# Kernel optimization log

Measured on AMD Instinct MI355X. Metric: run time of the kernel, lower is better.

The kernel has to match this reference:

```python
import jax, jax.numpy as jnp
import numpy as np

B, S, D_IN, D_OUT, H = 4, 2048, 1024, 1024, 16
HD = D_OUT // H


def setup_inputs() -> dict:
    key = jax.random.key(0)
    ks = jax.random.split(key, 6)
    s_in = 1.0 / np.sqrt(D_IN)
    s_out = 1.0 / np.sqrt(D_OUT)
    return {
        "x": jax.random.normal(ks[0], (B, S, D_IN), dtype=jnp.float32),
        "Wq": jax.random.uniform(ks[1], (D_IN, D_OUT), jnp.float32, -s_in, s_in),
        "Wk": jax.random.uniform(ks[2], (D_IN, D_OUT), jnp.float32, -s_in, s_in),
        "Wv": jax.random.uniform(ks[3], (D_IN, D_OUT), jnp.float32, -s_in, s_in),
        "Wo": jax.random.uniform(ks[4], (D_OUT, D_OUT), jnp.float32, -s_out, s_out),
        "bo": jax.random.uniform(ks[5], (D_OUT,), jnp.float32, -s_out, s_out),
    }


def reference(x, Wq, Wk, Wv, Wo, bo):
    b, s, _ = x.shape
    # project and split heads: (b, h, s, hd)
    def heads(w):
        return (x @ w).reshape(b, s, H, HD).transpose(0, 2, 1, 3)
    q, k, v = heads(Wq), heads(Wk), heads(Wv)
    scores = jnp.einsum("bhqd,bhkd->bhqk", q, k) / np.sqrt(HD).astype(np.float32)
    causal = jnp.tril(jnp.ones((s, s), dtype=bool))  # True = keep
    scores = jnp.where(causal, scores, -jnp.inf)
    attn = jax.nn.softmax(scores, axis=-1)
    ctx = jnp.einsum("bhqk,bhkd->bhqd", attn, v)
    ctx = ctx.transpose(0, 2, 1, 3).reshape(b, s, D_OUT)
    return ctx @ Wo.T + bo
```

## Files before the change

kernel.cpp:

```cpp
#include <hip/hip_runtime.h>
#include <hip/hip_bf16.h>

#define BB   4
#define SS   2048
#define DIN  1024
#define DOUT 1024
#define NH   16
#define HDIM 64

typedef __hip_bfloat16 bf16;
typedef __attribute__((ext_vector_type(8))) short short8;
typedef __attribute__((ext_vector_type(4))) float floatx4;

#define AS1(p) ((const __attribute__((address_space(1))) void*)(p))
#define AS3(p) ((__attribute__((address_space(3))) void*)(p))

__global__ void cast_f32_bf16_kernel(const float* __restrict__ src, bf16* __restrict__ dst) {
    size_t i = ((size_t)blockIdx.x * 256 + threadIdx.x) * 8;
    float4 a = *(const float4*)(src + i);
    float4 b = *(const float4*)(src + i + 4);
    bf16 o[8] __attribute__((aligned(16)));
    o[0] = __float2bfloat16(a.x); o[1] = __float2bfloat16(a.y);
    o[2] = __float2bfloat16(a.z); o[3] = __float2bfloat16(a.w);
    o[4] = __float2bfloat16(b.x); o[5] = __float2bfloat16(b.y);
    o[6] = __float2bfloat16(b.z); o[7] = __float2bfloat16(b.w);
    *(short8*)(dst + i) = *(short8*)o;
}

__global__ void prep_wqkv_kernel(const float* __restrict__ Wq, const float* __restrict__ Wk,
                                 const float* __restrict__ Wv, bf16* __restrict__ wt) {
    __shared__ float tile[64][65];
    const int kt = blockIdx.x;
    const int nt = blockIdx.y;
    const int k0 = kt * 64, n0 = nt * 64;
    const float* W = (n0 < 1024) ? Wq : (n0 < 2048 ? Wk : Wv);
    const int col0 = n0 & 1023;
    const int tid = threadIdx.x;
    {
        const int kl = tid >> 2, nc = (tid & 3) * 16;
        const float* src = W + (size_t)(k0 + kl) * 1024 + col0 + nc;
        #pragma unroll
        for (int i = 0; i < 16; i += 4) {
            float4 v = *(const float4*)(src + i);
            tile[kl][nc + i + 0] = v.x; tile[kl][nc + i + 1] = v.y;
            tile[kl][nc + i + 2] = v.z; tile[kl][nc + i + 3] = v.w;
        }
    }
    __syncthreads();
    {
        const int nl = tid >> 2, kc = (tid & 3) * 16;
        bf16 o[16] __attribute__((aligned(16)));
        #pragma unroll
        for (int i = 0; i < 16; ++i) o[i] = __float2bfloat16(tile[kc + i][nl]);
        bf16* dst = wt + (size_t)(n0 + nl) * 1024 + k0 + kc;
        *(short8*)dst       = *(short8*)&o[0];
        *(short8*)(dst + 8) = *(short8*)&o[8];
    }
}

template<int EPI>
__global__ __launch_bounds__(256) void gemm_bt_kernel(
    const bf16* __restrict__ A, const bf16* __restrict__ Bt,
    void* __restrict__ C, const float* __restrict__ bias, int K, int ldc) {
    __shared__ __align__(16) bf16 As[128][32];
    __shared__ __align__(16) bf16 Bs[128][32];
    const int tid  = threadIdx.x;
    const int wave = tid >> 6, lane = tid & 63;
    const int lm   = lane & 15, quad = lane >> 4;
    const int wm   = (wave >> 1) * 64, wn = (wave & 1) * 64;
    const size_t rowA0 = (size_t)blockIdx.x * 128;
    const size_t rowB0 = (size_t)blockIdx.y * 128;
    const int srow = wave * 16 + (lane >> 2);
    const int skc  = (lane & 3) * 8;

    floatx4 acc[4][4] = {};

    for (int k0 = 0; k0 < K; k0 += 32) {
        __syncthreads();
        #pragma unroll
        for (int r = 0; r < 2; ++r) {
            const bf16* gA = A  + (rowA0 + r * 64 + srow) * (size_t)K + k0 + skc;
            __builtin_amdgcn_global_load_lds(AS1(gA), AS3(&As[r * 64 + wave * 16][0]), 16, 0, 0);
            const bf16* gB = Bt + (rowB0 + r * 64 + srow) * (size_t)K + k0 + skc;
            __builtin_amdgcn_global_load_lds(AS1(gB), AS3(&Bs[r * 64 + wave * 16][0]), 16, 0, 0);
        }
        __syncthreads();
        short8 a[4], b[4];
        #pragma unroll
        for (int i = 0; i < 4; ++i) a[i] = *(const short8*)&As[wm + i * 16 + lm][quad * 8];
        #pragma unroll
        for (int j = 0; j < 4; ++j) b[j] = *(const short8*)&Bs[wn + j * 16 + lm][quad * 8];
        #pragma unroll
        for (int i = 0; i < 4; ++i)
            #pragma unroll
            for (int j = 0; j < 4; ++j)
                acc[i][j] = __builtin_amdgcn_mfma_f32_16x16x32_bf16(a[i], b[j], acc[i][j], 0, 0, 0);
    }

    #pragma unroll
    for (int i = 0; i < 4; ++i) {
        size_t row = rowA0 + wm + i * 16 + quad * 4;
        #pragma unroll
        for (int j = 0; j < 4; ++j) {
            size_t col = rowB0 + wn + j * 16 + lm;
            float bv = (EPI == 1) ? bias[col] : 0.0f;
            #pragma unroll
            for (int r = 0; r < 4; ++r) {
                if (EPI == 0)
                    ((bf16*)C)[(row + r) * ldc + col] = __float2bfloat16(acc[i][j][r]);
                else
                    ((float*)C)[(row + r) * ldc + col] = acc[i][j][r] + bv;
            }
        }
    }
}

__global__ void transpose_v_kernel(const bf16* __restrict__ qkv, bf16* __restrict__ vt) {
    __shared__ __align__(16) bf16 tile[64][72];
    const int st = blockIdx.x;
    const int bh = blockIdx.y;
    const int b = bh >> 4, h = bh & 15;
    const int s0 = st * 64;
    const int tid = threadIdx.x;
    {
        const int sl = tid >> 2, hc = (tid & 3) * 16;
        const bf16* src = qkv + ((size_t)(b * SS + s0 + sl)) * 3072 + 2048 + h * 64 + hc;
        *(short8*)&tile[sl][hc]     = *(const short8*)src;
        *(short8*)&tile[sl][hc + 8] = *(const short8*)(src + 8);
    }
    __syncthreads();
    {
        const int hl = tid >> 2, sc = (tid & 3) * 16;
        bf16 o[16] __attribute__((aligned(16)));
        #pragma unroll
        for (int i = 0; i < 16; ++i) o[i] = tile[sc + i][hl];
        bf16* dst = vt + ((size_t)(bh * 64 + hl)) * SS + s0 + sc;
        *(short8*)dst       = *(short8*)&o[0];
        *(short8*)(dst + 8) = *(short8*)&o[8];
    }
}

#define PSTR 68
__global__ __launch_bounds__(256, 2) void flash_attn_kernel(
    const bf16* __restrict__ qkv, const bf16* __restrict__ vt, bf16* __restrict__ ctx) {
    __shared__ __align__(16) bf16 Ks[64 * 64];
    __shared__ __align__(16) bf16 Vs[64 * 64];
    __shared__ __align__(16) bf16 Pl[4][32 * PSTR + 8];
    const int tid  = threadIdx.x;
    const int wave = tid >> 6, lane = tid & 63;
    const int lm   = lane & 15, quad = lane >> 4;

    const int id  = blockIdx.x;
    const int j   = id >> 3;
    const int bh  = (id & 7) * 8 + (j & 7);
    const int p0  = j >> 3;
    const int b = bh >> 4, h = bh & 15;

    const int lane8r = lane >> 3;
    const int schunk = (lane & 7) ^ lane8r;

    bf16* Pw = &Pl[wave][0];

    #pragma unroll 1
    for (int ph = 0; ph < 2; ++ph) {
        const int p = ph ? (15 - p0) : p0;
        const int qb = p * 128 + wave * 32;
        const int nkt = 2 * p + 2;

        short8 bq[2][2];
        #pragma unroll
        for (int g = 0; g < 2; ++g) {
            const bf16* qp = qkv + ((size_t)(b * SS + qb + g * 16 + lm)) * 3072 + h * 64 + quad * 8;
            bq[g][0] = *(const short8*)qp;
            bq[g][1] = *(const short8*)(qp + 32);
        }

        floatx4 o[2][4] = {};
        float lsum[2] = {0.f, 0.f};

        #pragma unroll 1
        for (int kt = 0; kt < nkt; ++kt) {
            __syncthreads();
            #pragma unroll
            for (int c = 0; c < 2; ++c) {
                const int row = c * 32 + wave * 8 + lane8r;
                const bf16* gk = qkv + ((size_t)(b * SS + kt * 64 + row)) * 3072 + 1024 + h * 64 + schunk * 8;
                __builtin_amdgcn_global_load_lds(AS1(gk), AS3(Ks + (c * 256 + wave * 64) * 8), 16, 0, 0);
                const bf16* gv = vt + ((size_t)((b * NH + h) * 64 + row)) * SS + kt * 64 + schunk * 8;
                __builtin_amdgcn_global_load_lds(AS1(gv), AS3(Vs + (c * 256 + wave * 64) * 8), 16, 0, 0);
            }
            __syncthreads();

            const int sw = lm & 7;
            short8 ka[4][2], va[4][2];
            #pragma unroll
            for (int nt = 0; nt < 4; ++nt) {
                const int r0 = (nt * 16 + lm) * 64;
                ka[nt][0] = *(const short8*)(Ks + r0 + ((quad ^ sw) * 8));
                ka[nt][1] = *(const short8*)(Ks + r0 + (((4 + quad) ^ sw) * 8));
                va[nt][0] = *(const short8*)(Vs + r0 + ((quad ^ sw) * 8));
                va[nt][1] = *(const short8*)(Vs + r0 + (((4 + quad) ^ sw) * 8));
            }

            #pragma unroll
            for (int g = 0; g < 2; ++g) {
                floatx4 sc[4];
                #pragma unroll
                for (int nt = 0; nt < 4; ++nt) {
                    floatx4 z = {};
                    z = __builtin_amdgcn_mfma_f32_16x16x32_bf16(ka[nt][0], bq[g][0], z, 0, 0, 0);
                    z = __builtin_amdgcn_mfma_f32_16x16x32_bf16(ka[nt][1], bq[g][1], z, 0, 0, 0);
                    sc[nt] = z;
                }
                if (kt * 64 + 63 > qb + g * 16) {
                    const int qrow = qb + g * 16 + lm;
                    #pragma unroll
                    for (int nt = 0; nt < 4; ++nt)
                        #pragma unroll
                        for (int r = 0; r < 4; ++r)
                            if (kt * 64 + nt * 16 + quad * 4 + r > qrow) sc[nt][r] = -1e30f;
                }
                #pragma unroll
                for (int nt = 0; nt < 4; ++nt) {
                    bf16 pk[4] __attribute__((aligned(8)));
                    #pragma unroll
                    for (int r = 0; r < 4; ++r) {
                        float pv = __builtin_amdgcn_exp2f(sc[nt][r] * 0.18033688f);
                        lsum[g] += pv;
                        pk[r] = __float2bfloat16(pv);
                    }
                    *(uint64_t*)&Pw[(g * 16 + lm) * PSTR + nt * 16 + quad * 4] = *(uint64_t*)pk;
                }
            }
            #pragma unroll
            for (int g = 0; g < 2; ++g) {
                const short8 ap0 = *(const short8*)&Pw[(g * 16 + lm) * PSTR + quad * 8];
                const short8 ap1 = *(const short8*)&Pw[(g * 16 + lm) * PSTR + 32 + quad * 8];
                #pragma unroll
                for (int t = 0; t < 4; ++t) {
                    o[g][t] = __builtin_amdgcn_mfma_f32_16x16x32_bf16(ap0, va[t][0], o[g][t], 0, 0, 0);
                    o[g][t] = __builtin_amdgcn_mfma_f32_16x16x32_bf16(ap1, va[t][1], o[g][t], 0, 0, 0);
                }
            }
        }

        #pragma unroll
        for (int g = 0; g < 2; ++g) {
            float rsum = lsum[g];
            rsum += __shfl_xor(rsum, 16);
            rsum += __shfl_xor(rsum, 32);
            float rl[4];
            #pragma unroll
            for (int r = 0; r < 4; ++r) rl[r] = 1.0f / __shfl(rsum, quad * 4 + r);
            #pragma unroll
            for (int t = 0; t < 4; ++t)
                #pragma unroll
                for (int r = 0; r < 4; ++r) {
                    size_t row = (size_t)b * SS + qb + g * 16 + quad * 4 + r;
                    ctx[row * 1024 + h * 64 + t * 16 + lm] = __float2bfloat16(o[g][t][r] * rl[r]);
                }
        }
    }
}

extern "C" void kernel_launch(void* const* d_in, const int* in_sizes, int n_in,
                              void* d_out, int out_size, void* d_ws, size_t ws_size,
                              hipStream_t stream) {
    const float* x  = (const float*)d_in[0];
    const float* Wq = (const float*)d_in[1];
    const float* Wk = (const float*)d_in[2];
    const float* Wv = (const float*)d_in[3];
    const float* Wo = (const float*)d_in[4];
    const float* bo = (const float*)d_in[5];

    char* ws = (char*)d_ws;
    bf16* xb  = (bf16*)ws;  ws += (size_t)8192 * 1024 * 2;
    bf16* wt  = (bf16*)ws;  ws += (size_t)3072 * 1024 * 2;
    bf16* wob = (bf16*)ws;  ws += (size_t)1024 * 1024 * 2;
    bf16* qkv = (bf16*)ws;  ws += (size_t)8192 * 3072 * 2;
    bf16* vtb = (bf16*)ws;  ws += (size_t)BB * NH * HDIM * SS * 2;
    bf16* ctx = xb;

    cast_f32_bf16_kernel<<<4096, 256, 0, stream>>>(x, xb);
    prep_wqkv_kernel<<<dim3(16, 48), 256, 0, stream>>>(Wq, Wk, Wv, wt);
    cast_f32_bf16_kernel<<<512, 256, 0, stream>>>(Wo, wob);
    gemm_bt_kernel<0><<<dim3(64, 24), 256, 0, stream>>>(xb, wt, (void*)qkv, nullptr, 1024, 3072);
    transpose_v_kernel<<<dim3(32, 64), 256, 0, stream>>>(qkv, vtb);
    flash_attn_kernel<<<512, 256, 0, stream>>>(qkv, vtb, ctx);
    gemm_bt_kernel<1><<<dim3(64, 8), 256, 0, stream>>>(ctx, wob, d_out, bo, 1024, 1024);
}
```

Before: 273.5 us.

## Double-buffer K/V tiles in LDS and prefetch next tile during compute

Adds a second LDS buffer for the K and V tiles in the flash attention kernel. The first tile is loaded before the loop, and each iteration issues async global-to-LDS loads for the next tile before computing on the current one. This hides global load latency behind the MFMA work and drops one barrier per iteration. In exchange it doubles K/V LDS usage and relies on the compiler placing the correct wait counters before the barrier for the async LDS loads.

```diff
diff --git a/kernel.cpp b/kernel.cpp
--- a/kernel.cpp
+++ b/kernel.cpp
@@ -143,8 +143,8 @@
 #define PSTR 68
 __global__ __launch_bounds__(256, 2) void flash_attn_kernel(
     const bf16* __restrict__ qkv, const bf16* __restrict__ vt, bf16* __restrict__ ctx) {
-    __shared__ __align__(16) bf16 Ks[64 * 64];
-    __shared__ __align__(16) bf16 Vs[64 * 64];
+    __shared__ __align__(16) bf16 Ks[2][64 * 64];
+    __shared__ __align__(16) bf16 Vs[2][64 * 64];
     __shared__ __align__(16) bf16 Pl[4][32 * PSTR + 8];
     const int tid  = threadIdx.x;
     const int wave = tid >> 6, lane = tid & 63;
@@ -159,6 +159,9 @@
     const int lane8r = lane >> 3;
     const int schunk = (lane & 7) ^ lane8r;
 
+    const bf16* kg = qkv + (size_t)b * SS * 3072 + 1024 + h * 64 + schunk * 8;
+    const bf16* vg = vt + (size_t)(b * NH + h) * 64 * SS + schunk * 8;
+
     bf16* Pw = &Pl[wave][0];
 
     #pragma unroll 1
@@ -178,28 +181,40 @@
         floatx4 o[2][4] = {};
         float lsum[2] = {0.f, 0.f};
 
+        if (ph) __syncthreads();
+        #pragma unroll
+        for (int c = 0; c < 2; ++c) {
+            const int row = c * 32 + wave * 8 + lane8r;
+            __builtin_amdgcn_global_load_lds(AS1(kg + (size_t)row * 3072), AS3(&Ks[0][(c * 256 + wave * 64) * 8]), 16, 0, 0);
+            __builtin_amdgcn_global_load_lds(AS1(vg + (size_t)row * SS), AS3(&Vs[0][(c * 256 + wave * 64) * 8]), 16, 0, 0);
+        }
+
         #pragma unroll 1
         for (int kt = 0; kt < nkt; ++kt) {
+            const int cur = kt & 1;
             __syncthreads();
-            #pragma unroll
-            for (int c = 0; c < 2; ++c) {
-                const int row = c * 32 + wave * 8 + lane8r;
-                const bf16* gk = qkv + ((size_t)(b * SS + kt * 64 + row)) * 3072 + 1024 + h * 64 + schunk * 8;
-                __builtin_amdgcn_global_load_lds(AS1(gk), AS3(Ks + (c * 256 + wave * 64) * 8), 16, 0, 0);
-                const bf16* gv = vt + ((size_t)((b * NH + h) * 64 + row)) * SS + kt * 64 + schunk * 8;
-                __builtin_amdgcn_global_load_lds(AS1(gv), AS3(Vs + (c * 256 + wave * 64) * 8), 16, 0, 0);
-            }
-            __syncthreads();
+            if (kt + 1 < nkt) {
+                #pragma unroll
+                for (int c = 0; c < 2; ++c) {
+                    const int row = c * 32 + wave * 8 + lane8r;
+                    __builtin_amdgcn_global_load_lds(AS1(kg + (size_t)((kt + 1) * 64 + row) * 3072),
+                                                     AS3(&Ks[cur ^ 1][(c * 256 + wave * 64) * 8]), 16, 0, 0);
+                    __builtin_amdgcn_global_load_lds(AS1(vg + (size_t)row * SS + (kt + 1) * 64),
+                                                     AS3(&Vs[cur ^ 1][(c * 256 + wave * 64) * 8]), 16, 0, 0);
+                }
+            }
 
             const int sw = lm & 7;
+            const bf16* Ksb = &Ks[cur][0];
+            const bf16* Vsb = &Vs[cur][0];
             short8 ka[4][2], va[4][2];
             #pragma unroll
             for (int nt = 0; nt < 4; ++nt) {
                 const int r0 = (nt * 16 + lm) * 64;
-                ka[nt][0] = *(const short8*)(Ks + r0 + ((quad ^ sw) * 8));
-                ka[nt][1] = *(const short8*)(Ks + r0 + (((4 + quad) ^ sw) * 8));
-                va[nt][0] = *(const short8*)(Vs + r0 + ((quad ^ sw) * 8));
-                va[nt][1] = *(const short8*)(Vs + r0 + (((4 + quad) ^ sw) * 8));
+                ka[nt][0] = *(const short8*)(Ksb + r0 + ((quad ^ sw) * 8));
+                ka[nt][1] = *(const short8*)(Ksb + r0 + (((4 + quad) ^ sw) * 8));
+                va[nt][0] = *(const short8*)(Vsb + r0 + ((quad ^ sw) * 8));
+                va[nt][1] = *(const short8*)(Vsb + r0 + (((4 + quad) ^ sw) * 8));
             }
 
             #pragma unroll
```

After: 273.1 us. No clear change (-0.2%).
